# Kernel optimization log

Measured on AMD Instinct MI355X. Metric: run time of the kernel, lower is better.

## Reference

```python
import jax, jax.numpy as jnp
import numpy as np

TAU = 10.0      # LIFNode tau (hard-coded in REClipper)
V_TH = 1.0      # spikingjelly default v_threshold
ALPHA = 2.0     # surrogate.ATan default alpha

@jax.custom_vjp
def heaviside(x):
    return (x >= 0.0).astype(x.dtype)

def _h_fwd(x):
    return heaviside(x), x

def _h_bwd(x, g):
    # ATan surrogate gradient: alpha/2 / (1 + (pi/2 * alpha * x)^2)
    return (g * (ALPHA / 2.0) / (1.0 + (jnp.pi / 2.0 * ALPHA * x) ** 2),)

heaviside.defvjp(_h_fwd, _h_bwd)

def lif_scan(x_seq):
    # x_seq: [S, C, H, W]; LIF with decay_input=True, hard reset to 0.
    def step(v, x):
        v = v + (x - v) / TAU          # charge
        s = heaviside(v - V_TH)        # fire
        v = v * (1.0 - s)              # hard reset (v_reset = 0)
        return v, s
    v0 = jnp.zeros_like(x_seq[0])
    _, spikes = jax.lax.scan(step, v0, x_seq)
    return spikes

def conv3x3(x, w, b=None):
    y = jax.lax.conv_general_dilated(x, w, (1, 1), 'SAME',
                                     dimension_numbers=('NCHW', 'OIHW', 'NCHW'))
    if b is not None:
        y = y + b[None, :, None, None]
    return y

def encoder(ev, w1, w2):
    # ev: [B, T, 1, H, W]. Original loops sample-by-sample WITHOUT resetting the
    # LIF state between samples, so the membrane state carries over B*T steps.
    B, T, C, H, W = ev.shape
    s = lif_scan(ev.reshape(B * T, C, H, W))   # [B*T, 1, H, W] spikes
    y = jax.nn.relu(conv3x3(s, w1))            # [B*T, 4, H, W]
    y = jax.nn.relu(conv3x3(y, w2))            # [B*T, 1, H, W]
    # mean over T then mean over B == mean over flattened B*T
    return y.mean(0)                           # [1, H, W]

def setup_inputs() -> dict:
    key = jax.random.key(0)
    ks = jax.random.split(key, 11)
    B, T, H, W = 4, 16, 512, 512
    C_OUT = 32
    f = jnp.float32
    return {
        'On_event':  jax.random.uniform(ks[0], (B, T, 1, H, W), dtype=f),
        'Off_event': jax.random.uniform(ks[1], (B, T, 1, H, W), dtype=f),
        'rgb':       jax.random.uniform(ks[2], (1, 3, H, W), dtype=f),
        'on_w1':  jax.random.normal(ks[3], (4, 1, 3, 3), dtype=f) * 0.3,
        'on_w2':  jax.random.normal(ks[4], (1, 4, 3, 3), dtype=f) * 0.3,
        'off_w1': jax.random.normal(ks[5], (4, 1, 3, 3), dtype=f) * 0.3,
        'off_w2': jax.random.normal(ks[6], (1, 4, 3, 3), dtype=f) * 0.3,
        'clip_w1': jax.random.normal(ks[7], (16, 5, 3, 3), dtype=f) * 0.1,
        'clip_b1': jnp.zeros((16,), dtype=f),
        'clip_w2': jax.random.normal(ks[8], (C_OUT, 16, 3, 3), dtype=f) * 0.1,
        'clip_b2': jnp.zeros((C_OUT,), dtype=f),
    }

def reference(On_event, Off_event, rgb, on_w1, on_w2, off_w1, off_w2,
              clip_w1, clip_b1, clip_w2, clip_b2):
    On = encoder(On_event, on_w1, on_w2)[None]    # [1, 1, H, W]
    Off = encoder(Off_event, off_w1, off_w2)[None]
    x = jnp.concatenate([On, Off, rgb], axis=1)   # [1, 5, H, W]
    x = jax.nn.relu(conv3x3(x, clip_w1, clip_b1)) # [1, 16, H, W]
    x = jax.nn.relu(conv3x3(x, clip_w2, clip_b2)) # [1, C_out, H, W]
    return x
```

## Files before the change

### kernel.cpp

```cpp
#include <hip/hip_runtime.h>
#include <stdint.h>

#define IMW 512
#define HW 262144

typedef unsigned long long ull;
typedef __attribute__((ext_vector_type(4))) float f32x4;
typedef __attribute__((ext_vector_type(8))) _Float16 h8;

__global__ __launch_bounds__(256) void k0_rearrange(
    const float* __restrict__ cw2, const float* __restrict__ cw1,
    _Float16* __restrict__ w2h, float* __restrict__ w1r) {
  int i = blockIdx.x * 256 + threadIdx.x;
  if (i < 5120) {
    int oc = i / 160, k = i % 160;
    int tap = k >> 4, ic = k & 15;
    float v = (tap < 9) ? cw2[oc * 144 + ic * 9 + tap] : 0.0f;
    w2h[i] = (_Float16)v;
  }
  if (i < 720) {
    int oc = i / 45, tap = i % 45;
    w1r[tap * 16 + oc] = cw1[i];
  }
}

__global__ __launch_bounds__(256) void k1_lif(
    const float* __restrict__ on, const float* __restrict__ off,
    ull* __restrict__ R) {
  int enc = blockIdx.z;
  const float* ev = enc ? off : on;
  int wv = threadIdx.x >> 6;
  int lane = threadIdx.x & 63;
  int row = blockIdx.y;
  const float* p = ev + (size_t)row * IMW + wv * 128 + lane;
  float v0 = 0.f, v1 = 0.f;
  ull keep0 = 0, keep1 = 0;
#pragma unroll
  for (int t = 0; t < 64; ++t) {
    const float* q = p + (size_t)t * HW;
    float x0 = q[0];
    float x1 = q[64];
    v0 = fmaf(x0 - v0, 0.1f, v0);
    v1 = fmaf(x1 - v1, 0.1f, v1);
    bool s0 = (v0 >= 1.0f);
    bool s1 = (v1 >= 1.0f);
    ull b0 = __ballot(s0);
    ull b1 = __ballot(s1);
    if (s0) v0 = 0.f;
    if (s1) v1 = 0.f;
    keep0 = (lane == t) ? b0 : keep0;
    keep1 = (lane == t) ? b1 : keep1;
  }
  ull* dst = R + (((size_t)enc * 64 + lane) * IMW + row) * 8 + wv * 2;
  dst[0] = keep0;
  dst[1] = keep1;
}

__global__ __launch_bounds__(256) void k2_enc(
    const ull* __restrict__ R, const float* __restrict__ on_w1,
    const float* __restrict__ on_w2, const float* __restrict__ off_w1,
    const float* __restrict__ off_w2, float* __restrict__ means) {
  __shared__ ull spk[64][8][2];
  __shared__ float4 t1v[512];
  int tid = threadIdx.x;
  int enc = blockIdx.z;
  int wcb = blockIdx.x;
  int r0 = blockIdx.y * 4;
  ull any = 0;
#pragma unroll
  for (int i = 0; i < 2; ++i) {
    int pair = tid * 2 + i;
    int t = pair >> 3, row = pair & 7;
    int gy = r0 - 2 + row;
    ull Wp = 0, Wc = 0, Wn = 0;
    if (gy >= 0 && gy < IMW) {
      const ull* base = R + (((size_t)enc * 64 + t) * IMW + gy) * 8;
      Wc = base[wcb];
      if (wcb > 0) Wp = base[wcb - 1];
      if (wcb < 7) Wn = base[wcb + 1];
    }
    spk[t][row][0] = (Wc << 2) | (Wp >> 62);
    spk[t][row][1] = (Wc >> 2) | (Wn << 62);
    any |= Wp | Wc | Wn;
  }
  int lane = tid & 63, wv = tid >> 6;
  int c = wcb * 64 + lane;
  int r = r0 + wv;
  float* outp = means + (size_t)enc * HW + r * IMW + c;
  int nz = __syncthreads_or(any != 0ull);
  if (!nz) { *outp = 0.0f; return; }

  const float* w1 = enc ? off_w1 : on_w1;
  const float* w2 = enc ? off_w2 : on_w2;
#pragma unroll
  for (int i = 0; i < 2; ++i) {
    int e = tid + 256 * i;
    float a0 = 0.f, a1 = 0.f, a2 = 0.f, a3 = 0.f;
#pragma unroll
    for (int k = 0; k < 9; ++k) {
      if (e & (1 << k)) {
        a0 += w1[k]; a1 += w1[9 + k]; a2 += w1[18 + k]; a3 += w1[27 + k];
      }
    }
    t1v[e] = make_float4(fmaxf(a0, 0.f), fmaxf(a1, 0.f),
                         fmaxf(a2, 0.f), fmaxf(a3, 0.f));
  }
  __syncthreads();
  float w2g[36];
#pragma unroll
  for (int i = 0; i < 36; ++i) w2g[i] = w2[i];
  float fm[9];
#pragma unroll
  for (int qi = 0; qi < 3; ++qi)
#pragma unroll
    for (int dx = 0; dx < 3; ++dx) {
      int q = r - 1 + qi, xp = c - 1 + dx;
      fm[qi * 3 + dx] =
          (q >= 0 && q < IMW && xp >= 0 && xp < IMW) ? 1.0f : 0.0f;
    }
  int selB = (lane >= 60) ? 1 : 0;
  int shamt = selB ? lane - 4 : lane;
  float acc = 0.0f;
  for (int t = 0; t < 64; ++t) {
    unsigned r5[5];
#pragma unroll
    for (int k = 0; k < 5; ++k)
      r5[k] = (unsigned)((spk[t][wv + k][selB] >> shamt) & 31ull);
    float sum = 0.0f;
#pragma unroll
    for (int qi = 0; qi < 3; ++qi) {
#pragma unroll
      for (int dx = 0; dx < 3; ++dx) {
        unsigned pat = ((r5[qi] >> dx) & 7u) |
                       (((r5[qi + 1] >> dx) & 7u) << 3) |
                       (((r5[qi + 2] >> dx) & 7u) << 6);
        float4 sv = t1v[pat];
        int j = qi * 3 + dx;
        float d = w2g[j] * sv.x + w2g[9 + j] * sv.y + w2g[18 + j] * sv.z +
                  w2g[27 + j] * sv.w;
        sum = fmaf(fm[j], d, sum);
      }
    }
    acc += fmaxf(sum, 0.0f);
  }
  *outp = acc * (1.0f / 64.0f);
}

__global__ __launch_bounds__(256) void k3_clip(
    const float* __restrict__ means, const float* __restrict__ rgb,
    const float* __restrict__ w1r, const float* __restrict__ b1,
    const _Float16* __restrict__ w2h, const float* __restrict__ b2,
    float* __restrict__ out) {
  __shared__ __align__(16) float xs[5][12][68];
  __shared__ __align__(16) _Float16 stage[660 * 16];
  int tid = threadIdx.x;
  int c0 = blockIdx.x * 64;
  int r0 = blockIdx.y * 8;
#pragma unroll
  for (int k = 0; k < 16; ++k) {
    int idx = tid + 256 * k;
    if (idx < 4080) {
      int ch = idx / 816, rem = idx % 816;
      int row = rem / 68, col = rem % 68;
      int gy = r0 - 2 + row, gx = c0 - 2 + col;
      float val = 0.0f;
      if (gy >= 0 && gy < IMW && gx >= 0 && gx < IMW) {
        val = (ch < 2) ? means[(size_t)ch * HW + gy * IMW + gx]
                       : rgb[(size_t)(ch - 2) * HW + gy * IMW + gx];
      }
      xs[ch][row][col] = val;
    }
  }
  __syncthreads();
#pragma unroll 1
  for (int rep = 0; rep < 3; ++rep) {
    int p = tid + (rep << 8);
    if (p < 660) {
      int sr = p / 66, sc = p % 66;
      float a[16];
#pragma unroll
      for (int oc = 0; oc < 16; ++oc) a[oc] = b1[oc];
#pragma unroll 1
      for (int ic = 0; ic < 5; ++ic) {
        const float* xp = &xs[ic][sr][sc];
#pragma unroll
        for (int dy = 0; dy < 3; ++dy) {
#pragma unroll
          for (int dx = 0; dx < 3; ++dx) {
            float x = xp[dy * 68 + dx];
            const float* wrow = w1r + (ic * 9 + dy * 3 + dx) * 16;
#pragma unroll
            for (int oc = 0; oc < 16; ++oc)
              a[oc] = fmaf(wrow[oc], x, a[oc]);
          }
        }
      }
      int q = r0 - 1 + sr, gxp = c0 - 1 + sc;
      float msk =
          (q >= 0 && q < IMW && gxp >= 0 && gxp < IMW) ? 1.0f : 0.0f;
      unsigned w[8];
#pragma unroll
      for (int j = 0; j < 8; ++j) {
        unsigned lo = (unsigned)__builtin_bit_cast(
            unsigned short, (_Float16)(msk * fmaxf(a[2 * j], 0.f)));
        unsigned hi = (unsigned)__builtin_bit_cast(
            unsigned short, (_Float16)(msk * fmaxf(a[2 * j + 1], 0.f)));
        w[j] = lo | (hi << 16);
      }
      uint4* dst = (uint4*)((char*)stage + p * 32);
      dst[0] = make_uint4(w[0], w[1], w[2], w[3]);
      dst[1] = make_uint4(w[4], w[5], w[6], w[7]);
    }
  }
  __syncthreads();
  int og = __builtin_amdgcn_readfirstlane(tid >> 6);
  int lane = tid & 63;
  int xl = lane & 15;
  int quad = lane >> 4;
  int ichalf = quad & 1;
  int q2 = quad >> 1;
  int myoff[5];
#pragma unroll
  for (int c = 0; c < 5; ++c) {
    int tap = 2 * c + q2;
    if (tap > 8) tap = 8;
    myoff[c] = ((tap / 3) * 66 + (tap % 3)) * 32;
  }
  h8 bf[5][2];
  const char* wb = (const char*)w2h;
#pragma unroll
  for (int c = 0; c < 5; ++c) {
#pragma unroll
    for (int nt = 0; nt < 2; ++nt) {
      int oc = nt * 16 + xl;
      f32x4 t = *(const f32x4*)(wb + oc * 320 + c * 64 + quad * 16);
      bf[c][nt] = __builtin_bit_cast(h8, t);
    }
  }
  float bias0 = b2[xl];
  float bias1 = b2[16 + xl];
#pragma unroll 1
  for (int mi = 0; mi < 8; ++mi) {
    int m = og * 8 + mi;
    int py = m >> 2;
    int x0 = (m & 3) << 4;
    int bb = ((py * 66 + x0 + xl) << 5) + (ichalf << 4);
    f32x4 acc0 = {0.f, 0.f, 0.f, 0.f};
    f32x4 acc1 = {0.f, 0.f, 0.f, 0.f};
#pragma unroll
    for (int c = 0; c < 5; ++c) {
      f32x4 ar = *(const f32x4*)((const char*)stage + bb + myoff[c]);
      h8 af = __builtin_bit_cast(h8, ar);
      acc0 = __builtin_amdgcn_mfma_f32_16x16x32_f16(af, bf[c][0], acc0, 0, 0, 0);
      acc1 = __builtin_amdgcn_mfma_f32_16x16x32_f16(af, bf[c][1], acc1, 0, 0, 0);
    }
    int px = c0 + x0 + ((lane >> 4) << 2);
    float* o0 = out + (size_t)xl * HW + (r0 + py) * IMW + px;
    float* o1 = o0 + (size_t)16 * HW;
    *(float4*)o0 = make_float4(fmaxf(acc0[0] + bias0, 0.f),
                               fmaxf(acc0[1] + bias0, 0.f),
                               fmaxf(acc0[2] + bias0, 0.f),
                               fmaxf(acc0[3] + bias0, 0.f));
    *(float4*)o1 = make_float4(fmaxf(acc1[0] + bias1, 0.f),
                               fmaxf(acc1[1] + bias1, 0.f),
                               fmaxf(acc1[2] + bias1, 0.f),
                               fmaxf(acc1[3] + bias1, 0.f));
  }
}

extern "C" void kernel_launch(void* const* d_in, const int* in_sizes, int n_in,
                              void* d_out, int out_size, void* d_ws,
                              size_t ws_size, hipStream_t stream) {
  const float* on_ev  = (const float*)d_in[0];
  const float* off_ev = (const float*)d_in[1];
  const float* rgb    = (const float*)d_in[2];
  const float* on_w1  = (const float*)d_in[3];
  const float* on_w2  = (const float*)d_in[4];
  const float* off_w1 = (const float*)d_in[5];
  const float* off_w2 = (const float*)d_in[6];
  const float* cw1    = (const float*)d_in[7];
  const float* cb1    = (const float*)d_in[8];
  const float* cw2    = (const float*)d_in[9];
  const float* cb2    = (const float*)d_in[10];
  float* out = (float*)d_out;
  char* ws = (char*)d_ws;
  ull* R = (ull*)ws;
  float* means = (float*)(ws + (4u << 20));
  float* w1r = (float*)(ws + (6u << 20));
  _Float16* w2h = (_Float16*)(ws + (6u << 20) + (16u << 10));

  hipLaunchKernelGGL(k0_rearrange, dim3(20), dim3(256), 0, stream,
                     cw2, cw1, w2h, w1r);
  hipLaunchKernelGGL(k1_lif, dim3(1, 512, 2), dim3(256), 0, stream,
                     on_ev, off_ev, R);
  hipLaunchKernelGGL(k2_enc, dim3(8, 128, 2), dim3(256), 0, stream,
                     R, on_w1, on_w2, off_w1, off_w2, means);
  hipLaunchKernelGGL(k3_clip, dim3(8, 64), dim3(256), 0, stream,
                     means, rgb, w1r, cb1, w2h, cb2, out);
}
```

Baseline: 63.18 us.

## Store per-pixel 64-bit spike histories and transpose to row masks in encoder

```diff
diff --git a/kernel.cpp b/kernel.cpp
--- a/kernel.cpp
+++ b/kernel.cpp
@@ -26,40 +26,43 @@
 
 __global__ __launch_bounds__(256) void k1_lif(
     const float* __restrict__ on, const float* __restrict__ off,
-    ull* __restrict__ R) {
+    ull* __restrict__ R2) {
   int enc = blockIdx.z;
   const float* ev = enc ? off : on;
-  int wv = threadIdx.x >> 6;
-  int lane = threadIdx.x & 63;
   int row = blockIdx.y;
-  const float* p = ev + (size_t)row * IMW + wv * 128 + lane;
-  float v0 = 0.f, v1 = 0.f;
-  ull keep0 = 0, keep1 = 0;
-#pragma unroll
-  for (int t = 0; t < 64; ++t) {
-    const float* q = p + (size_t)t * HW;
-    float x0 = q[0];
-    float x1 = q[64];
-    v0 = fmaf(x0 - v0, 0.1f, v0);
-    v1 = fmaf(x1 - v1, 0.1f, v1);
-    bool s0 = (v0 >= 1.0f);
-    bool s1 = (v1 >= 1.0f);
-    ull b0 = __ballot(s0);
-    ull b1 = __ballot(s1);
-    if (s0) v0 = 0.f;
-    if (s1) v1 = 0.f;
-    keep0 = (lane == t) ? b0 : keep0;
-    keep1 = (lane == t) ? b1 : keep1;
-  }
-  ull* dst = R + (((size_t)enc * 64 + lane) * IMW + row) * 8 + wv * 2;
-  dst[0] = keep0;
-  dst[1] = keep1;
+  int x = blockIdx.x * 256 + threadIdx.x;
+  const float* p = ev + (size_t)row * IMW + x;
+  float v = 0.0f;
+  unsigned hlo = 0, hhi = 0;
+  float buf[16];
+#pragma unroll
+  for (int j = 0; j < 8; ++j) buf[j] = p[(size_t)j * HW];
+#pragma unroll
+  for (int batch = 0; batch < 8; ++batch) {
+    if (batch < 7) {
+#pragma unroll
+      for (int j = 0; j < 8; ++j)
+        buf[(((batch + 1) & 1) << 3) + j] = p[(size_t)((batch + 1) * 8 + j) * HW];
+    }
+#pragma unroll
+    for (int j = 0; j < 8; ++j) {
+      int t = batch * 8 + j;
+      float xv = buf[((batch & 1) << 3) + j];
+      v = fmaf(xv - v, 0.1f, v);
+      bool s = (v >= 1.0f);
+      if (s) v = 0.0f;
+      if (t < 32) hlo |= s ? (1u << t) : 0u;
+      else        hhi |= s ? (1u << (t - 32)) : 0u;
+    }
+  }
+  R2[((size_t)enc * IMW + row) * IMW + x] = ((ull)hhi << 32) | hlo;
 }
 
 __global__ __launch_bounds__(256) void k2_enc(
-    const ull* __restrict__ R, const float* __restrict__ on_w1,
+    const ull* __restrict__ R2, const float* __restrict__ on_w1,
     const float* __restrict__ on_w2, const float* __restrict__ off_w1,
     const float* __restrict__ off_w2, float* __restrict__ means) {
+  __shared__ ull hist[8][68];
   __shared__ ull spk[64][8][2];
   __shared__ float4 t1v[512];
   int tid = threadIdx.x;
@@ -68,20 +71,17 @@
   int r0 = blockIdx.y * 4;
   ull any = 0;
 #pragma unroll
-  for (int i = 0; i < 2; ++i) {
-    int pair = tid * 2 + i;
-    int t = pair >> 3, row = pair & 7;
-    int gy = r0 - 2 + row;
-    ull Wp = 0, Wc = 0, Wn = 0;
-    if (gy >= 0 && gy < IMW) {
-      const ull* base = R + (((size_t)enc * 64 + t) * IMW + gy) * 8;
-      Wc = base[wcb];
-      if (wcb > 0) Wp = base[wcb - 1];
-      if (wcb < 7) Wn = base[wcb + 1];
-    }
-    spk[t][row][0] = (Wc << 2) | (Wp >> 62);
-    spk[t][row][1] = (Wc >> 2) | (Wn << 62);
-    any |= Wp | Wc | Wn;
+  for (int rep = 0; rep < 3; ++rep) {
+    int idx = tid + 256 * rep;
+    if (idx < 544) {
+      int row = idx / 68, col = idx % 68;
+      int gy = r0 - 2 + row, gx = wcb * 64 - 2 + col;
+      ull h = 0;
+      if (gy >= 0 && gy < IMW && gx >= 0 && gx < IMW)
+        h = R2[((size_t)enc * IMW + gy) * IMW + gx];
+      hist[row][col] = h;
+      any |= h;
+    }
   }
   int lane = tid & 63, wv = tid >> 6;
   int c = wcb * 64 + lane;
@@ -90,6 +90,17 @@
   int nz = __syncthreads_or(any != 0ull);
   if (!nz) { *outp = 0.0f; return; }
 
+#pragma unroll 1
+  for (int r2 = 0; r2 < 2; ++r2) {
+    int row = wv * 2 + r2;
+    ull hA = hist[row][lane];
+    ull hB = hist[row][lane + 4];
+    for (int t = 0; t < 64; ++t) {
+      ull wA = __ballot((unsigned)((hA >> t) & 1ull));
+      ull wB = __ballot((unsigned)((hB >> t) & 1ull));
+      if (lane == t) { spk[t][row][0] = wA; spk[t][row][1] = wB; }
+    }
+  }
   const float* w1 = enc ? off_w1 : on_w1;
   const float* w2 = enc ? off_w2 : on_w2;
 #pragma unroll
@@ -284,17 +295,17 @@
   const float* cb2    = (const float*)d_in[10];
   float* out = (float*)d_out;
   char* ws = (char*)d_ws;
-  ull* R = (ull*)ws;
+  ull* R2 = (ull*)ws;
   float* means = (float*)(ws + (4u << 20));
   float* w1r = (float*)(ws + (6u << 20));
   _Float16* w2h = (_Float16*)(ws + (6u << 20) + (16u << 10));
 
   hipLaunchKernelGGL(k0_rearrange, dim3(20), dim3(256), 0, stream,
                      cw2, cw1, w2h, w1r);
-  hipLaunchKernelGGL(k1_lif, dim3(1, 512, 2), dim3(256), 0, stream,
-                     on_ev, off_ev, R);
+  hipLaunchKernelGGL(k1_lif, dim3(2, 512, 2), dim3(256), 0, stream,
+                     on_ev, off_ev, R2);
   hipLaunchKernelGGL(k2_enc, dim3(8, 128, 2), dim3(256), 0, stream,
-                     R, on_w1, on_w2, off_w1, off_w2, means);
+                     R2, on_w1, on_w2, off_w1, off_w2, means);
   hipLaunchKernelGGL(k3_clip, dim3(8, 64), dim3(256), 0, stream,
                      means, rgb, w1r, cb1, w2h, cb2, out);
 }
```

Result: faster. 56.72 us (-10.2%).
